# Optimization experiments

Measured on AMD Instinct MI355X. Metric: run time of the kernel, lower is better.

Reference implementation:

```python
import jax, jax.numpy as jnp
import numpy as np

K = 31  # AvgPool2d kernel size
P = 15  # padding


def _box_avg(x):
    """31x31 stride-1 avg pool, count_include_pad=True (PyTorch default):
    separable ones-conv with zero padding, divided by K*K."""
    B, C, H, W = x.shape
    kh = jnp.ones((C, 1, K, 1), x.dtype)
    kw = jnp.ones((C, 1, 1, K), x.dtype)
    dn = ('NCHW', 'OIHW', 'NCHW')
    y = jax.lax.conv_general_dilated(x, kh, (1, 1), [(P, P), (0, 0)],
                                     dimension_numbers=dn, feature_group_count=C)
    y = jax.lax.conv_general_dilated(y, kw, (1, 1), [(0, 0), (P, P)],
                                     dimension_numbers=dn, feature_group_count=C)
    return y / (K * K)


def setup_inputs() -> dict:
    key = jax.random.key(0)
    k1, k2 = jax.random.split(key)
    pred = jax.random.normal(k1, (64, 1, 512, 512), dtype=jnp.float32)
    mask = jax.random.uniform(k2, (64, 1, 512, 512), dtype=jnp.float32)
    return {"pred": pred, "mask": mask}


def reference(pred, mask):
    weit = 1.0 + 5.0 * jnp.abs(_box_avg(mask) - mask)
    p = jax.nn.sigmoid(pred)
    inter = jnp.sum(p * mask * weit, axis=(2, 3))          # [B, C]
    union = jnp.sum((p + mask) * weit, axis=(2, 3))        # [B, C]
    wdiss = 1.0 - (2.0 * inter + 0.5) / (union + 0.5)
    return jnp.mean(wdiss)
```

## Files before the change

kernel.cpp:

```cpp
#include <hip/hip_runtime.h>
#include <math.h>

#define NB 64
#define HH 512
#define WW 512
#define KK 31
#define PP 15
#define TS 32
#define NSTRIP (HH / TS)
#define HR (TS + KK - 1)

typedef _Float16 f16;
typedef f16 f16x8 __attribute__((ext_vector_type(8)));
typedef f16 f16x4 __attribute__((ext_vector_type(4)));


__global__ __launch_bounds__(512, 4) void dice_fused_kernel(
        const float* __restrict__ pred,
        const float* __restrict__ mask,
        float* __restrict__ part) {
    const int strip = blockIdx.x;
    const int b     = blockIdx.y;
    const int t     = threadIdx.x;
    const int wave  = t >> 6;
    const int lane  = t & 63;

    __shared__ f16 Hs[HR][WW];
    __shared__ float red[16];

    const float* mb = mask + (size_t)b * HH * WW;
    const float* pb = pred + (size_t)b * HH * WW;
    const int y0 = strip * TS;

    const int xbase = lane * 8;
    #pragma unroll
    for (int k = 0; k < 8; ++k) {
        const int r = k * 8 + wave;
        if (r >= HR) break;
        const int gy = y0 + r - PP;
        if (gy < 0 || gy >= HH) {
            f16x8 z = {(f16)0, (f16)0, (f16)0, (f16)0, (f16)0, (f16)0, (f16)0, (f16)0};
            *(f16x8*)&Hs[r][xbase] = z;
            continue;
        }
        const float* row = mb + (size_t)gy * WW;
        const float4 a  = *(const float4*)(row + xbase);
        const float4 bb = *(const float4*)(row + xbase + 4);

        float s0 = a.x;
        float s1 = s0 + a.y;
        float s2 = s1 + a.z;
        float s3 = s2 + a.w;
        float s4 = s3 + bb.x;
        float s5 = s4 + bb.y;
        float s6 = s5 + bb.z;
        float s7 = s6 + bb.w;

        float incl = s7;
        #pragma unroll
        for (int off = 1; off < 64; off <<= 1) {
            float tt = __shfl_up(incl, off);
            if (lane >= off) incl += tt;
        }
        const float base = incl - s7;
        s0 += base; s1 += base; s2 += base; s3 += base;
        s4 += base; s5 += base; s6 += base; s7 += base;

        const float total = __shfl(incl, 63);

        float hiv[8], lov[8];
        hiv[0] = __shfl_down(s7, 1);
        hiv[1] = __shfl_down(s0, 2);
        hiv[2] = __shfl_down(s1, 2);
        hiv[3] = __shfl_down(s2, 2);
        hiv[4] = __shfl_down(s3, 2);
        hiv[5] = __shfl_down(s4, 2);
        hiv[6] = __shfl_down(s5, 2);
        hiv[7] = __shfl_down(s6, 2);
        lov[0] = __shfl_up(s0, 2);
        lov[1] = __shfl_up(s1, 2);
        lov[2] = __shfl_up(s2, 2);
        lov[3] = __shfl_up(s3, 2);
        lov[4] = __shfl_up(s4, 2);
        lov[5] = __shfl_up(s5, 2);
        lov[6] = __shfl_up(s6, 2);
        lov[7] = __shfl_up(s7, 2);

        f16x8 hv;
        #pragma unroll
        for (int j = 0; j < 8; ++j) {
            const int x = xbase + j;
            const float mhi = (x + PP > WW - 1) ? total : hiv[j];
            const float mlo = (x - PP - 1 >= 0) ? lov[j] : 0.0f;
            hv[j] = (f16)(mhi - mlo);
        }
        *(f16x8*)&Hs[r][xbase] = hv;
    }
    __syncthreads();

    const int q  = t & 127;
    const int g  = t >> 7;
    const int c  = q * 4;
    const int r0 = g * 8;

    float4 B = make_float4(0.f, 0.f, 0.f, 0.f);
    #pragma unroll
    for (int j = 0; j < KK - 1; ++j) {
        const f16x4 h = *(const f16x4*)&Hs[r0 + j][c];
        B.x += (float)h[0]; B.y += (float)h[1]; B.z += (float)h[2]; B.w += (float)h[3];
    }

    float4 I4 = make_float4(0.f, 0.f, 0.f, 0.f);
    float4 U4 = make_float4(0.f, 0.f, 0.f, 0.f);
    const float inv2 = 1.0f / (float)(KK * KK);

    #pragma unroll
    for (int i = 0; i < 8; ++i) {
        const int y = y0 + r0 + i;
        const f16x4 he = *(const f16x4*)&Hs[r0 + i + (KK - 1)][c];
        const f16x4 hl = *(const f16x4*)&Hs[r0 + i][c];
        const float4 m4 = *(const float4*)(mb + (size_t)y * WW + c);
        const float4 p4 = *(const float4*)(pb + (size_t)y * WW + c);

        B.x += (float)he[0]; B.y += (float)he[1]; B.z += (float)he[2]; B.w += (float)he[3];

        const float w0 = 1.0f + 5.0f * fabsf(B.x * inv2 - m4.x);
        const float w1 = 1.0f + 5.0f * fabsf(B.y * inv2 - m4.y);
        const float w2 = 1.0f + 5.0f * fabsf(B.z * inv2 - m4.z);
        const float w3 = 1.0f + 5.0f * fabsf(B.w * inv2 - m4.w);
        const float sg0 = 1.0f / (1.0f + __expf(-p4.x));
        const float sg1 = 1.0f / (1.0f + __expf(-p4.y));
        const float sg2 = 1.0f / (1.0f + __expf(-p4.z));
        const float sg3 = 1.0f / (1.0f + __expf(-p4.w));

        I4.x += sg0 * m4.x * w0;  U4.x += (sg0 + m4.x) * w0;
        I4.y += sg1 * m4.y * w1;  U4.y += (sg1 + m4.y) * w1;
        I4.z += sg2 * m4.z * w2;  U4.z += (sg2 + m4.z) * w2;
        I4.w += sg3 * m4.w * w3;  U4.w += (sg3 + m4.w) * w3;

        B.x -= (float)hl[0]; B.y -= (float)hl[1]; B.z -= (float)hl[2]; B.w -= (float)hl[3];
    }

    float inter = I4.x + I4.y + I4.z + I4.w;
    float uni   = U4.x + U4.y + U4.z + U4.w;
    #pragma unroll
    for (int off = 32; off > 0; off >>= 1) {
        inter += __shfl_down(inter, off);
        uni   += __shfl_down(uni, off);
    }
    if (lane == 0) { red[wave] = inter; red[8 + wave] = uni; }
    __syncthreads();
    if (t == 0) {
        float ti = 0.f, tu = 0.f;
        #pragma unroll
        for (int w2 = 0; w2 < 8; ++w2) { ti += red[w2]; tu += red[8 + w2]; }
        const int bid = b * NSTRIP + strip;
        part[bid] = ti;
        part[NB * NSTRIP + bid] = tu;
    }
}

__global__ void dice_final_kernel(const float* __restrict__ part,
                                  float* __restrict__ out) {
    const int t = threadIdx.x;
    float inter = 0.0f, uni = 0.0f;
    #pragma unroll
    for (int s = 0; s < NSTRIP; ++s) {
        inter += part[t * NSTRIP + s];
        uni   += part[NB * NSTRIP + t * NSTRIP + s];
    }
    float wd = 1.0f - (2.0f * inter + 0.5f) / (uni + 0.5f);
    #pragma unroll
    for (int off = 32; off > 0; off >>= 1) wd += __shfl_down(wd, off);
    if (t == 0) out[0] = wd * (1.0f / (float)NB);
}

extern "C" void kernel_launch(void* const* d_in, const int* in_sizes, int n_in,
                              void* d_out, int out_size, void* d_ws, size_t ws_size,
                              hipStream_t stream) {
    const float* pred = (const float*)d_in[0];
    const float* mask = (const float*)d_in[1];
    float* out  = (float*)d_out;
    float* part = (float*)d_ws;

    dim3 grid(NSTRIP, NB);
    dice_fused_kernel<<<grid, 512, 0, stream>>>(pred, mask, part);
    dice_final_kernel<<<1, 64, 0, stream>>>(part, out);
}
```

Baseline: 152.6 us.

## Replace full-row prefix scan with local windowed sums packed as fp16 pairs

The horizontal box-sum no longer runs a 64-lane prefix scan per row. Each lane now builds its 31-wide window from its own 8-element partial sums plus those of its neighbours at distances 1 and 2, fetched with a few shuffles. Two rows are handled together by packing their values into f16x2, so each shuffle and add serves both rows. This removes the log-step scan and halves shuffle traffic. In exchange the window sums are accumulated in fp16 rather than fp32, which adds rounding error on sums of up to 31 values.

```diff
diff --git a/kernel.cpp b/kernel.cpp
--- a/kernel.cpp
+++ b/kernel.cpp
@@ -9,10 +9,25 @@
 #define TS 32
 #define NSTRIP (HH / TS)
 #define HR (TS + KK - 1)
+#define NPAIR (HR / 2)
 
 typedef _Float16 f16;
 typedef f16 f16x8 __attribute__((ext_vector_type(8)));
 typedef f16 f16x4 __attribute__((ext_vector_type(4)));
+typedef f16 f16x2 __attribute__((ext_vector_type(2)));
+
+__device__ __forceinline__ f16x2 shfl_up2(f16x2 v, int delta) {
+    int x = __shfl_up(__builtin_bit_cast(int, v), delta);
+    return __builtin_bit_cast(f16x2, x);
+}
+__device__ __forceinline__ f16x2 shfl_dn2(f16x2 v, int delta) {
+    int x = __shfl_down(__builtin_bit_cast(int, v), delta);
+    return __builtin_bit_cast(f16x2, x);
+}
+__device__ __forceinline__ f16x2 sel2(bool c, f16x2 v) {
+    f16x2 z = {(f16)0, (f16)0};
+    return c ? v : z;
+}
 
 
 __global__ __launch_bounds__(512, 4) void dice_fused_kernel(
@@ -33,68 +48,76 @@
     const int y0 = strip * TS;
 
     const int xbase = lane * 8;
-    #pragma unroll
-    for (int k = 0; k < 8; ++k) {
-        const int r = k * 8 + wave;
-        if (r >= HR) break;
-        const int gy = y0 + r - PP;
-        if (gy < 0 || gy >= HH) {
-            f16x8 z = {(f16)0, (f16)0, (f16)0, (f16)0, (f16)0, (f16)0, (f16)0, (f16)0};
-            *(f16x8*)&Hs[r][xbase] = z;
-            continue;
+    const bool lm1 = (lane >= 1);
+    const bool lm2 = (lane >= 2);
+    const bool lp1 = (lane <= 62);
+    const bool lp2 = (lane <= 61);
+
+    #pragma unroll
+    for (int k = 0; k < 4; ++k) {
+        const int p = k * 8 + wave;
+        if (p >= NPAIR) continue;
+        const int ra = 2 * p;
+        const int rb = ra + 1;
+        const int gya = y0 + ra - PP;
+        const int gyb = gya + 1;
+
+        float va[8], vb[8];
+        if (gya >= 0 && gya < HH) {
+            const float* row = mb + (size_t)gya * WW + xbase;
+            const float4 u = *(const float4*)(row);
+            const float4 v = *(const float4*)(row + 4);
+            va[0] = u.x; va[1] = u.y; va[2] = u.z; va[3] = u.w;
+            va[4] = v.x; va[5] = v.y; va[6] = v.z; va[7] = v.w;
+        } else {
+            #pragma unroll
+            for (int j = 0; j < 8; ++j) va[j] = 0.0f;
         }
-        const float* row = mb + (size_t)gy * WW;
-        const float4 a  = *(const float4*)(row + xbase);
-        const float4 bb = *(const float4*)(row + xbase + 4);
-
-        float s0 = a.x;
-        float s1 = s0 + a.y;
-        float s2 = s1 + a.z;
-        float s3 = s2 + a.w;
-        float s4 = s3 + bb.x;
-        float s5 = s4 + bb.y;
-        float s6 = s5 + bb.z;
-        float s7 = s6 + bb.w;
-
-        float incl = s7;
-        #pragma unroll
-        for (int off = 1; off < 64; off <<= 1) {
-            float tt = __shfl_up(incl, off);
-            if (lane >= off) incl += tt;
+        if (gyb >= 0 && gyb < HH) {
+            const float* row = mb + (size_t)gyb * WW + xbase;
+            const float4 u = *(const float4*)(row);
+            const float4 v = *(const float4*)(row + 4);
+            vb[0] = u.x; vb[1] = u.y; vb[2] = u.z; vb[3] = u.w;
+            vb[4] = v.x; vb[5] = v.y; vb[6] = v.z; vb[7] = v.w;
+        } else {
+            #pragma unroll
+            for (int j = 0; j < 8; ++j) vb[j] = 0.0f;
         }
-        const float base = incl - s7;
-        s0 += base; s1 += base; s2 += base; s3 += base;
-        s4 += base; s5 += base; s6 += base; s7 += base;
-
-        const float total = __shfl(incl, 63);
-
-        float hiv[8], lov[8];
-        hiv[0] = __shfl_down(s7, 1);
-        hiv[1] = __shfl_down(s0, 2);
-        hiv[2] = __shfl_down(s1, 2);
-        hiv[3] = __shfl_down(s2, 2);
-        hiv[4] = __shfl_down(s3, 2);
-        hiv[5] = __shfl_down(s4, 2);
-        hiv[6] = __shfl_down(s5, 2);
-        hiv[7] = __shfl_down(s6, 2);
-        lov[0] = __shfl_up(s0, 2);
-        lov[1] = __shfl_up(s1, 2);
-        lov[2] = __shfl_up(s2, 2);
-        lov[3] = __shfl_up(s3, 2);
-        lov[4] = __shfl_up(s4, 2);
-        lov[5] = __shfl_up(s5, 2);
-        lov[6] = __shfl_up(s6, 2);
-        lov[7] = __shfl_up(s7, 2);
-
-        f16x8 hv;
+
+        float sa[8], sb[8];
+        sa[0] = va[0]; sb[0] = vb[0];
+        #pragma unroll
+        for (int j = 1; j < 8; ++j) { sa[j] = sa[j-1] + va[j]; sb[j] = sb[j-1] + vb[j]; }
+
+        f16x2 ps[8];
+        #pragma unroll
+        for (int j = 0; j < 8; ++j) { ps[j][0] = (f16)sa[j]; ps[j][1] = (f16)sb[j]; }
+        const f16x2 pT = ps[7];
+
+        f16x2 A[7];
+        #pragma unroll
+        for (int j = 0; j < 7; ++j) A[j] = shfl_up2(pT - ps[j], 2);
+        const f16x2 Bprev = shfl_up2(pT, 1);
+        const f16x2 Cfull = shfl_dn2(pT, 1);
+        f16x2 Cp[7];
+        #pragma unroll
+        for (int j = 0; j < 7; ++j) Cp[j] = shfl_dn2(ps[j], 2);
+
+        f16x2 base = pT;
+        base += sel2(lm1, Bprev);
+        base += sel2(lp1, Cfull);
+
+        f16x8 ha, hb;
         #pragma unroll
         for (int j = 0; j < 8; ++j) {
-            const int x = xbase + j;
-            const float mhi = (x + PP > WW - 1) ? total : hiv[j];
-            const float mlo = (x - PP - 1 >= 0) ? lov[j] : 0.0f;
-            hv[j] = (f16)(mhi - mlo);
+            f16x2 acc = base;
+            if (j < 7) acc += sel2(lm2, A[j]);
+            if (j > 0) acc += sel2(lp2, Cp[j-1]);
+            ha[j] = acc[0];
+            hb[j] = acc[1];
         }
-        *(f16x8*)&Hs[r][xbase] = hv;
+        *(f16x8*)&Hs[ra][xbase] = ha;
+        *(f16x8*)&Hs[rb][xbase] = hb;
     }
     __syncthreads();
 
```

After: 151.7 us. Within noise of the previous version (-0.6%).
